# Performance work log

Hardware: AMD Instinct MI355X
Metric: run time of the kernel (lower is better)

The kernel has to match this reference:

```python
import jax, jax.numpy as jnp
import numpy as np

B, DIM, H, W = 8, 128, 128, 128
QK, MLP, HEADS, NT, GS = 128, 256, 4, 8, 128


def _ln(x, w, b):
    m = jnp.mean(x, -1, keepdims=True)
    v = jnp.mean((x - m) ** 2, -1, keepdims=True)
    return (x - m) * jax.lax.rsqrt(v + 1e-5) * w + b


def _norml2(x):
    n = jnp.sqrt(jnp.sum(x * x, -1, keepdims=True))
    return x / jnp.maximum(n, 1e-12)


def setup_inputs() -> dict:
    key = jax.random.key(0)
    ks = jax.random.split(key, 12)
    s = 0.02
    f32 = jnp.float32
    return {
        'x': jax.random.normal(ks[0], (B, DIM, H, W), f32),
        'means': jax.random.normal(ks[1], (NT, DIM), f32),
        'ln1_w': jnp.ones((DIM,), f32), 'ln1_b': jnp.zeros((DIM,), f32),
        'wq': jax.random.normal(ks[2], (QK, DIM), f32) * s,
        'wk': jax.random.normal(ks[3], (QK, DIM), f32) * s,
        'wv': jax.random.normal(ks[4], (DIM, DIM), f32) * s,
        'wproj': jax.random.normal(ks[5], (DIM, DIM), f32) * s,
        'irca_wk': jax.random.normal(ks[6], (QK, DIM), f32) * s,
        'irca_wv': jax.random.normal(ks[7], (DIM, DIM), f32) * s,
        'conv1x1_w': jax.random.normal(ks[8], (DIM, DIM), f32) * s,
        'ln2_w': jnp.ones((DIM,), f32), 'ln2_b': jnp.zeros((DIM,), f32),
        'fc1_w': jax.random.normal(ks[9], (MLP, DIM), f32) * s,
        'fc1_b': jnp.zeros((MLP,), f32),
        'dw_w': jax.random.normal(ks[10], (MLP, 1, 5, 5), f32) * s,
        'dw_b': jnp.zeros((MLP,), f32),
        'fc2_w': jax.random.normal(ks[11], (DIM, MLP), f32) * s,
        'fc2_b': jnp.zeros((DIM,), f32),
    }


def reference(x, means, ln1_w, ln1_b, wq, wk, wv, wproj, irca_wk, irca_wv,
              conv1x1_w, ln2_w, ln2_b, fc1_w, fc1_b, dw_w, dw_b, fc2_w, fc2_b):
    Bx, C, Hh, Ww = x.shape
    N = Hh * Ww
    xt = x.reshape(Bx, C, N).transpose(0, 2, 1)          # b n c
    residual = xt
    xn = _ln(xt, ln1_w, ln1_b)
    m = jax.lax.stop_gradient(means)                      # eval: means buffer, detached
    # IRCA (eval path): global K/V from cluster means
    dq, dv = QK // HEADS, C // HEADS
    kg = (m @ irca_wk.T).reshape(NT, HEADS, dq).transpose(1, 0, 2)  # h nt dq
    vg = (m @ irca_wv.T).reshape(NT, HEADS, dv).transpose(1, 0, 2)  # h nt dv
    # cluster assignment -> token reordering (no grad)
    scores = jnp.einsum('bic,jc->bij', _norml2(xn), _norml2(m))
    buckets = jnp.argmax(scores, axis=-1)
    idx = jnp.argsort(buckets, axis=-1)                   # [B,N] permutation
    # IASA
    q = xn @ wq.T
    k = xn @ wk.T
    v = xn @ wv.T
    take = lambda t: jnp.take_along_axis(t, idx[:, :, None], axis=1)
    q, k, v = take(q), take(k), take(v)
    gs = min(N, GS)
    ng = (N + gs - 1) // gs
    pad_n = ng * gs - N
    qp = jnp.concatenate([q, jnp.flip(q[:, N - pad_n:N], axis=1)], axis=1)
    qp = qp.reshape(Bx, ng, gs, HEADS, dq).transpose(0, 1, 3, 2, 4)  # b g h gs dq

    def window(t, d):
        tp = jnp.concatenate([t, jnp.flip(t[:, N - pad_n - gs:N], axis=1)], axis=1)
        blk = tp.reshape(Bx, ng + 1, gs, HEADS, d)
        win = jnp.concatenate([blk[:, :-1], blk[:, 1:]], axis=2)     # b g 2gs h d
        return win.transpose(0, 1, 3, 2, 4)

    kp = window(k, dq)
    vp = window(v, dv)
    scale = 1.0 / np.sqrt(dq)
    a1 = jax.nn.softmax(jnp.einsum('bghqd,bghkd->bghqk', qp, kp) * scale, axis=-1)
    out1 = jnp.einsum('bghqk,bghkd->bghqd', a1, vp)
    a2 = jax.nn.softmax(jnp.einsum('bghqd,hkd->bghqk', qp, kg) * scale, axis=-1)
    out2 = jnp.einsum('bghqk,hkd->bghqd', a2, vg)
    out = (out1 + out2).transpose(0, 1, 3, 2, 4).reshape(Bx, ng * gs, C)[:, :N]
    inv = jnp.argsort(idx, axis=-1)                       # scatter-back = inverse perm
    out = jnp.take_along_axis(out, inv[:, :, None], axis=1)
    out = out @ wproj.T
    yimg = out.transpose(0, 2, 1).reshape(Bx, C, Hh, Ww)
    yimg = jnp.einsum('oc,bchw->bohw', conv1x1_w, yimg)
    x2 = residual + yimg.reshape(Bx, C, N).transpose(0, 2, 1)
    # ConvFFN with PreNorm
    xm = _ln(x2, ln2_w, ln2_b)
    h1 = jax.nn.gelu(xm @ fc1_w.T + fc1_b, approximate=False)
    himg = h1.transpose(0, 2, 1).reshape(Bx, MLP, Hh, Ww)
    dwc = jax.lax.conv_general_dilated(himg, dw_w, (1, 1), 'SAME',
                                       feature_group_count=MLP,
                                       dimension_numbers=('NCHW', 'OIHW', 'NCHW'))
    dwc = jax.nn.gelu(dwc + dw_b.reshape(1, MLP, 1, 1), approximate=False)
    h1 = h1 + dwc.reshape(Bx, MLP, N).transpose(0, 2, 1)
    x3 = x2 + (h1 @ fc2_w.T + fc2_b)
    return x3.transpose(0, 2, 1).reshape(Bx, C, Hh, Ww)
```

## Files before the change

kernel.cpp:

```cpp
#include <hip/hip_runtime.h>
#include <math.h>

typedef unsigned short u16;
typedef unsigned int u32;
typedef __attribute__((ext_vector_type(8))) short bf16x8;
typedef __attribute__((ext_vector_type(4))) float f32x4;

constexpr int BB   = 8;
constexpr int DIMC = 128;
constexpr int HH   = 128;
constexpr int WW   = 128;
constexpr int NTOK = HH * WW;
constexpr int QKD  = 128;
constexpr int MLPD = 256;
constexpr int NTm  = 8;
constexpr int GSZ  = 128;
constexpr int NGRP = NTOK / GSZ;
constexpr size_t BIG = 16777216;

__device__ __forceinline__ float exp2_raw(float x) {
    return __builtin_amdgcn_exp2f(x);
}
__device__ __forceinline__ float gelu_f(float v) {
    float u = v * (0.7978845608028654f + 0.035677408136300125f * v * v);
    float e = exp2_raw(u * 2.885390081777927f);
    float th = 1.0f - 2.0f * __builtin_amdgcn_rcpf(e + 1.0f);
    return 0.5f * v * (1.0f + th);
}
__device__ __forceinline__ float b2f(u16 u) {
    return __uint_as_float(((u32)u) << 16);
}
__device__ __forceinline__ u16 f2b(float f) {
    u32 x = __float_as_uint(f);
    return (u16)((x + 0x7fffu + ((x >> 16) & 1u)) >> 16);
}
__device__ __forceinline__ float ulo(u32 u) { return __uint_as_float(u << 16); }
__device__ __forceinline__ float uhi(u32 u) { return __uint_as_float(u & 0xffff0000u); }

__global__ __launch_bounds__(128) void k_prep(const float* __restrict__ means,
        const float* __restrict__ iwk, const float* __restrict__ iwv,
        float* __restrict__ mhat, u16* __restrict__ kgbb, u16* __restrict__ vgtb) {
    __shared__ float sm[DIMC];
    __shared__ float inv_s;
    int tt = blockIdx.x;
    int t = threadIdx.x;
    sm[t] = means[tt * DIMC + t];
    __syncthreads();
    if (t == 0) {
        float s = 0.f;
        for (int c = 0; c < DIMC; c++) s += sm[c] * sm[c];
        inv_s = 1.f / fmaxf(sqrtf(s), 1e-12f);
    }
    __syncthreads();
    mhat[tt * DIMC + t] = sm[t] * inv_s;
    float sk = 0.f, sv = 0.f;
    #pragma unroll 8
    for (int c = 0; c < DIMC; c++) {
        sk = fmaf(sm[c], iwk[t * DIMC + c], sk);
        sv = fmaf(sm[c], iwv[t * DIMC + c], sv);
    }
    kgbb[tt * DIMC + t] = f2b(sk);
    vgtb[(t >> 5) * 256 + (t & 31) * 8 + tt] = f2b(sv);
}

__global__ __launch_bounds__(256) void k_cvtall(const float* __restrict__ wq,
        const float* __restrict__ wk, const float* __restrict__ wv,
        const float* __restrict__ fc1, const float* __restrict__ fc2,
        u16* __restrict__ wqkv, u16* __restrict__ fc1b, u16* __restrict__ fc2b) {
    int i = blockIdx.x * 256 + threadIdx.x;
    if (i < 49152) {
        const float* s = (i < 16384) ? wq : (i < 32768 ? wk : wv);
        wqkv[i] = f2b(s[i & 16383]);
    } else if (i < 81920) {
        fc1b[i - 49152] = f2b(fc1[i - 49152]);
    } else if (i < 114688) {
        fc2b[i - 81920] = f2b(fc2[i - 81920]);
    }
}

__global__ __launch_bounds__(256) void k_fuse(const float* __restrict__ c1,
        const float* __restrict__ wp, u16* __restrict__ wf) {
    __shared__ float wpS[DIMC * DIMC];
    int t = threadIdx.x;
    for (int i = t; i < DIMC * DIMC; i += 256) wpS[i] = wp[i];
    __syncthreads();
    int o = blockIdx.x * 2 + (t >> 7);
    int c = t & 127;
    float s = 0.f;
    #pragma unroll 8
    for (int m = 0; m < DIMC; m++) s = fmaf(c1[o * DIMC + m], wpS[m * DIMC + c], s);
    wf[o * DIMC + c] = f2b(s);
}

__global__ __launch_bounds__(256) void k_ln1(const float* __restrict__ x,
        const float* __restrict__ lw, const float* __restrict__ lb,
        const float* __restrict__ mhat, u16* __restrict__ xn, int* __restrict__ bucket) {
    __shared__ float smh[NTm * DIMC];
    __shared__ float lwb[DIMC], lbb[DIMC];
    __shared__ float red[4][64][3];
    __shared__ float scr[4][64][9];
    const int chunk = blockIdx.x;
    const int b = chunk >> 8;
    const int n0 = (chunk & 255) << 6;
    const int t = threadIdx.x;
    const int cg = t >> 6, tok = t & 63;
    const int n = n0 + tok;
    const int cbase = cg * 32;
    for (int i = t; i < NTm * DIMC; i += 256) smh[i] = mhat[i];
    if (t < DIMC) { lwb[t] = lw[t]; lbb[t] = lb[t]; }

    const float* xb = x + (size_t)b * DIMC * NTOK + (size_t)cbase * NTOK + n;
    float xv[32];
    float sum = 0.f, sq = 0.f;
    #pragma unroll
    for (int c = 0; c < 32; c++) {
        float v = xb[(size_t)c * NTOK];
        xv[c] = v;
        sum += v; sq += v * v;
    }
    red[cg][tok][0] = sum;
    red[cg][tok][1] = sq;
    __syncthreads();
    float s0 = red[0][tok][0] + red[1][tok][0] + red[2][tok][0] + red[3][tok][0];
    float q0 = red[0][tok][1] + red[1][tok][1] + red[2][tok][1] + red[3][tok][1];
    float mean = s0 * (1.0f / DIMC);
    float var = q0 * (1.0f / DIMC) - mean * mean;
    float rstd = rsqrtf(var + 1e-5f);

    float sc[NTm];
    #pragma unroll
    for (int j = 0; j < NTm; j++) sc[j] = 0.f;
    u32 opk[16];
    #pragma unroll
    for (int c = 0; c < 32; c += 2) {
        float v0 = (xv[c]     - mean) * rstd * lwb[cbase + c]     + lbb[cbase + c];
        float v1 = (xv[c + 1] - mean) * rstd * lwb[cbase + c + 1] + lbb[cbase + c + 1];
        #pragma unroll
        for (int j = 0; j < NTm; j++) {
            sc[j] = fmaf(v0, smh[j * DIMC + cbase + c], sc[j]);
            sc[j] = fmaf(v1, smh[j * DIMC + cbase + c + 1], sc[j]);
        }
        opk[c >> 1] = (u32)f2b(v0) | ((u32)f2b(v1) << 16);
    }
    u16* xnr = xn + ((size_t)b * NTOK + n) * DIMC + cbase;
    *(uint4*)(xnr + 0)  = make_uint4(opk[0],  opk[1],  opk[2],  opk[3]);
    *(uint4*)(xnr + 8)  = make_uint4(opk[4],  opk[5],  opk[6],  opk[7]);
    *(uint4*)(xnr + 16) = make_uint4(opk[8],  opk[9],  opk[10], opk[11]);
    *(uint4*)(xnr + 24) = make_uint4(opk[12], opk[13], opk[14], opk[15]);

    #pragma unroll
    for (int j = 0; j < NTm; j++) scr[cg][tok][j] = sc[j];
    __syncthreads();
    if (cg == 0) {
        float v0 = ((scr[0][tok][0] + scr[1][tok][0]) + (scr[2][tok][0] + scr[3][tok][0]));
        int best = 0; float bv = v0;
        #pragma unroll
        for (int j = 1; j < NTm; j++) {
            float v = ((scr[0][tok][j] + scr[1][tok][j]) + (scr[2][tok][j] + scr[3][tok][j]));
            if (v > bv) { bv = v; best = j; }
        }
        bucket[b * NTOK + n] = best;
    }
}

__global__ __launch_bounds__(64) void k_count(const int* __restrict__ bucket, int* __restrict__ cnt) {
    int chunk = blockIdx.x;
    int bk = bucket[(chunk << 6) + threadIdx.x];
    #pragma unroll
    for (int j = 0; j < NTm; j++) {
        unsigned long long m = __ballot(bk == j);
        if (threadIdx.x == 0) cnt[chunk * NTm + j] = (int)__popcll(m);
    }
}

__global__ __launch_bounds__(64) void k_scan(const int* __restrict__ cnt, int* __restrict__ base) {
    __shared__ int sc[256 * NTm];
    __shared__ int bb[NTm], tot[NTm];
    int b = blockIdx.x, t = threadIdx.x;
    for (int i = t; i < 256 * NTm; i += 64) sc[i] = cnt[b * 256 * NTm + i];
    __syncthreads();
    if (t < NTm) {
        int run = 0;
        for (int c = 0; c < 256; c++) {
            int v = sc[c * NTm + t];
            sc[c * NTm + t] = run;
            run += v;
        }
        tot[t] = run;
    }
    __syncthreads();
    if (t == 0) {
        int a = 0;
        for (int j = 0; j < NTm; j++) { bb[j] = a; a += tot[j]; }
    }
    __syncthreads();
    for (int i = t; i < 256 * NTm; i += 64) base[b * 256 * NTm + i] = sc[i] + bb[i & 7];
}

__global__ __launch_bounds__(64) void k_place(const int* __restrict__ bucket,
        const int* __restrict__ base, int* __restrict__ gidx) {
    int chunk = blockIdx.x;
    int lane = threadIdx.x;
    int nf = (chunk << 6) + lane;
    int bk = bucket[nf];
    unsigned long long lower = (1ull << lane) - 1ull;
    int rank = 0;
    #pragma unroll
    for (int j = 0; j < NTm; j++) {
        unsigned long long m = __ballot(bk == j);
        if (bk == j) rank = (int)__popcll(m & lower);
    }
    int b = nf >> 14;
    int pos = base[chunk * NTm + bk] + rank;
    gidx[b * NTOK + pos] = nf & (NTOK - 1);
}

__global__ __launch_bounds__(256) void k_inv(const int* __restrict__ gidx, u16* __restrict__ iinv) {
    int i = blockIdx.x * 256 + threadIdx.x;
    int b = i >> 14;
    iinv[((size_t)b << 14) + gidx[i]] = (u16)(i & (NTOK - 1));
}

template<int KDIM, int NOUT, int GATHER, int AIMG, int BIASF, int GELUF, int RES, int STIMG, int CBF, int LN2F>
__global__ __launch_bounds__(256) void g_mfma(const u16* __restrict__ A, const u16* __restrict__ W,
        const float* __restrict__ bias, const void* __restrict__ resid,
        const int* __restrict__ gidx, void* __restrict__ Cout, float ascale,
        const float* __restrict__ lnw, const float* __restrict__ lnb, void* __restrict__ Cout2) {
    __shared__ u16 As[128 * 40];
    __shared__ u16 Ws[128 * 40];
    const int b = blockIdx.z;
    const int m0 = blockIdx.x * 128;
    const int n0 = blockIdx.y * 128;
    const int t = threadIdx.x;
    const int lane = t & 63;
    const int wave = t >> 6;
    const int wm = (wave & 1) * 64;
    const int wn = (wave >> 1) * 64;
    const int srow = t >> 2;
    const int sko = (t & 3) * 8;
    const u16* pA0 = nullptr; const u16* pA1 = nullptr;
    if (!AIMG) {
        int ra0 = m0 + srow, ra1 = m0 + 64 + srow;
        if (GATHER == 1) {
            ra0 = gidx[b * NTOK + ra0];
            ra1 = gidx[b * NTOK + ra1];
        } else if (GATHER == 2) {
            const u16* gi = (const u16*)gidx;
            ra0 = gi[b * NTOK + ra0];
            ra1 = gi[b * NTOK + ra1];
        }
        pA0 = A + ((size_t)b * NTOK + ra0) * KDIM + sko;
        pA1 = A + ((size_t)b * NTOK + ra1) * KDIM + sko;
    }
    const u16* pW0 = W + (size_t)(n0 + srow) * KDIM + sko;
    const u16* pW1 = W + (size_t)(n0 + 64 + srow) * KDIM + sko;

    f32x4 acc[4][4];
    #pragma unroll
    for (int i = 0; i < 4; i++)
        #pragma unroll
        for (int j = 0; j < 4; j++) acc[i][j] = (f32x4){0.f, 0.f, 0.f, 0.f};

    uint4 a0c, a1c, w0c, w1c;
    u16 ec[16];
    if (!AIMG) {
        a0c = *(const uint4*)(pA0);
        a1c = *(const uint4*)(pA1);
    } else {
        const int kk2 = t & 31;
        const int tg = t >> 5;
        const u16* src = A + ((size_t)b * KDIM + kk2) * NTOK + m0 + tg * 16;
        *(uint4*)&ec[0] = *(const uint4*)src;
        *(uint4*)&ec[8] = *(const uint4*)(src + 8);
    }
    w0c = *(const uint4*)(pW0);
    w1c = *(const uint4*)(pW1);

    #pragma unroll
    for (int k0 = 0; k0 < KDIM; k0 += 32) {
        __syncthreads();
        if (!AIMG) {
            *(uint4*)&As[srow * 40 + sko] = a0c;
            *(uint4*)&As[(64 + srow) * 40 + sko] = a1c;
        } else {
            const int kk2 = t & 31;
            const int tg = t >> 5;
            #pragma unroll
            for (int j = 0; j < 16; j++) As[(tg * 16 + j) * 40 + kk2] = ec[j];
        }
        *(uint4*)&Ws[srow * 40 + sko] = w0c;
        *(uint4*)&Ws[(64 + srow) * 40 + sko] = w1c;
        __syncthreads();
        if (k0 + 32 < KDIM) {
            if (!AIMG) {
                a0c = *(const uint4*)(pA0 + k0 + 32);
                a1c = *(const uint4*)(pA1 + k0 + 32);
            } else {
                const int kk2 = t & 31;
                const int tg = t >> 5;
                const u16* src = A + ((size_t)b * KDIM + k0 + 32 + kk2) * NTOK + m0 + tg * 16;
                *(uint4*)&ec[0] = *(const uint4*)src;
                *(uint4*)&ec[8] = *(const uint4*)(src + 8);
            }
            w0c = *(const uint4*)(pW0 + k0 + 32);
            w1c = *(const uint4*)(pW1 + k0 + 32);
        }
        bf16x8 af[4], bfv[4];
        #pragma unroll
        for (int i = 0; i < 4; i++)
            af[i] = *(bf16x8*)&As[(wm + i * 16 + (lane & 15)) * 40 + (lane >> 4) * 8];
        #pragma unroll
        for (int j = 0; j < 4; j++)
            bfv[j] = *(bf16x8*)&Ws[(wn + j * 16 + (lane & 15)) * 40 + (lane >> 4) * 8];
        #pragma unroll
        for (int i = 0; i < 4; i++)
            #pragma unroll
            for (int j = 0; j < 4; j++)
                acc[i][j] = __builtin_amdgcn_mfma_f32_16x16x32_bf16(af[i], bfv[j], acc[i][j], 0, 0, 0);
    }

    const int c2 = lane & 15, gq2 = lane >> 4;
    int colj[4];
    #pragma unroll
    for (int j = 0; j < 4; j++) colj[j] = n0 + wn + j * 16 + c2;

    if (LN2F) {
        #pragma unroll
        for (int i = 0; i < 4; i++) {
            int rbase = m0 + wm + i * 16 + gq2 * 4;
            #pragma unroll
            for (int j = 0; j < 4; j++) {
                const float* rf = (const float*)resid;
                float4 rr = *(const float4*)&rf[((size_t)b * NOUT + colj[j]) * NTOK + rbase];
                acc[i][j][0] += rr.x; acc[i][j][1] += rr.y;
                acc[i][j][2] += rr.z; acc[i][j][3] += rr.w;
            }
        }
        __syncthreads();
        float* ps = (float*)&As[0];
        const int h = wn >> 6;
        float mean_[4][4], rstd_[4][4];
        #pragma unroll
        for (int i = 0; i < 4; i++)
            #pragma unroll
            for (int r = 0; r < 4; r++) {
                float s = 0.f, q = 0.f;
                #pragma unroll
                for (int j = 0; j < 4; j++) { float tv = acc[i][j][r]; s += tv; q += tv * tv; }
                s += __shfl_xor(s, 1, 64); q += __shfl_xor(q, 1, 64);
                s += __shfl_xor(s, 2, 64); q += __shfl_xor(q, 2, 64);
                s += __shfl_xor(s, 4, 64); q += __shfl_xor(q, 4, 64);
                s += __shfl_xor(s, 8, 64); q += __shfl_xor(q, 8, 64);
                if (c2 == 0) {
                    int rl = wm + i * 16 + gq2 * 4 + r;
                    ps[(h * 128 + rl) * 2 + 0] = s;
                    ps[(h * 128 + rl) * 2 + 1] = q;
                }
            }
        __syncthreads();
        #pragma unroll
        for (int i = 0; i < 4; i++)
            #pragma unroll
            for (int r = 0; r < 4; r++) {
                int rl = wm + i * 16 + gq2 * 4 + r;
                float s = ps[rl * 2 + 0] + ps[(128 + rl) * 2 + 0];
                float q = ps[rl * 2 + 1] + ps[(128 + rl) * 2 + 1];
                float mn = s * (1.0f / 128.0f);
                float vr = q * (1.0f / 128.0f) - mn * mn;
                mean_[i][r] = mn;
                rstd_[i][r] = rsqrtf(vr + 1e-5f);
            }
        float lwj[4], lbj[4];
        #pragma unroll
        for (int j = 0; j < 4; j++) { lwj[j] = lnw[colj[j]]; lbj[j] = lnb[colj[j]]; }
        u16* xo = (u16*)Cout;
        u16* mo = (u16*)Cout2;
        #pragma unroll
        for (int i = 0; i < 4; i++) {
            int rbase = m0 + wm + i * 16 + gq2 * 4;
            #pragma unroll
            for (int j = 0; j < 4; j++)
                #pragma unroll
                for (int r = 0; r < 4; r++) {
                    float tv = acc[i][j][r];
                    size_t off = ((size_t)b * NTOK + rbase + r) * NOUT + colj[j];
                    xo[off] = f2b(tv);
                    mo[off] = f2b((tv - mean_[i][r]) * rstd_[i][r] * lwj[j] + lbj[j]);
                }
        }
        return;
    }

    const float smul = (blockIdx.y == 0) ? ascale : 1.0f;
    float bj[4];
    #pragma unroll
    for (int j = 0; j < 4; j++) bj[j] = BIASF ? bias[colj[j]] : 0.f;
    #pragma unroll
    for (int i = 0; i < 4; i++) {
        int rbase = m0 + wm + i * 16 + gq2 * 4;
        #pragma unroll
        for (int j = 0; j < 4; j++) {
            f32x4 v = acc[i][j];
            v[0] *= smul; v[1] *= smul; v[2] *= smul; v[3] *= smul;
            if (BIASF) { v[0] += bj[j]; v[1] += bj[j]; v[2] += bj[j]; v[3] += bj[j]; }
            if (GELUF) { v[0] = gelu_f(v[0]); v[1] = gelu_f(v[1]); v[2] = gelu_f(v[2]); v[3] = gelu_f(v[3]); }
            if (RES == 1) {
                const float* rf = (const float*)resid;
                float4 rr = *(const float4*)&rf[((size_t)b * NOUT + colj[j]) * NTOK + rbase];
                v[0] += rr.x; v[1] += rr.y; v[2] += rr.z; v[3] += rr.w;
            } else if (RES == 3) {
                const u16* rb = (const u16*)resid;
                #pragma unroll
                for (int r = 0; r < 4; r++)
                    v[r] += b2f(rb[((size_t)b * NTOK + rbase + r) * NOUT + colj[j]]);
            }
            if (STIMG) {
                size_t off = ((size_t)b * NOUT + colj[j]) * NTOK + rbase;
                if (CBF) {
                    ushort4 o;
                    o.x = f2b(v[0]); o.y = f2b(v[1]); o.z = f2b(v[2]); o.w = f2b(v[3]);
                    *(ushort4*)((u16*)Cout + off) = o;
                } else {
                    *(float4*)((float*)Cout + off) = make_float4(v[0], v[1], v[2], v[3]);
                }
            } else {
                if (CBF) {
                    #pragma unroll
                    for (int r = 0; r < 4; r++)
                        ((u16*)Cout)[((size_t)b * NTOK + rbase + r) * NOUT + colj[j]] = f2b(v[r]);
                } else {
                    #pragma unroll
                    for (int r = 0; r < 4; r++)
                        ((float*)Cout)[((size_t)b * NTOK + rbase + r) * NOUT + colj[j]] = v[r];
                }
            }
        }
    }
}

__global__ __launch_bounds__(256, 3) void k_attn(const u16* __restrict__ qkv,
        const u16* __restrict__ kgbb, const u16* __restrict__ vgtb,
        u16* __restrict__ outp) {
    __shared__ u16 VT[2][32][264];
    __shared__ u16 Pb[4][64][32];
    const int g = blockIdx.x, hp = blockIdx.y, b = blockIdx.z;
    const int t = threadIdx.x;
    const int wave = t >> 6, lane = t & 63;
    const int c = lane & 15, gq = lane >> 4;
    const int lh = wave & 1, head = hp * 2 + lh, qh = wave >> 1;
    const size_t brow = (size_t)b * NTOK;
    const bool lastg = (g == NGRP - 1);
    const int csw = (c & 3) << 3;

    {
        int key = t;
        int pos = (!lastg || key < GSZ) ? g * GSZ + key : NTOK - 1 - (key - GSZ);
        const u16* vp = qkv + (brow + pos) * 384 + 256 + hp * 64;
        #pragma unroll
        for (int i = 0; i < 8; i++) {
            uint4 v = *(const uint4*)(vp + i * 8);
            u16 e[8];
            *(uint4*)e = v;
            #pragma unroll
            for (int j = 0; j < 8; j++) {
                int d = i * 8 + j;
                VT[d >> 5][d & 31][key] = e[j];
            }
        }
        if (t < 64) {
            int l2 = t >> 5, dv = t & 31;
            uint4 v = *(const uint4*)(vgtb + ((size_t)(hp * 2 + l2) * 32 + dv) * 8);
            *(uint4*)&VT[l2][dv][256] = v;
        }
    }

    const int q0 = g * GSZ + qh * 64;
    bf16x8 qf[4];
    #pragma unroll
    for (int nq = 0; nq < 4; nq++)
        qf[nq] = *(const bf16x8*)(qkv + (brow + q0 + nq * 16 + c) * 384 + head * 32 + gq * 8);

    const u16* kbp = qkv + brow * 384 + 128 + head * 32 + gq * 8;
    bf16x8 kfa[8][2];
    #pragma unroll
    for (int s = 0; s < 8; s++)
        #pragma unroll
        for (int mk = 0; mk < 2; mk++) {
            int kl = s * 32 + mk * 16 + c;
            int pos = (!lastg || kl < GSZ) ? g * GSZ + kl : NTOK - 1 - (kl - GSZ);
            kfa[s][mk] = *(const bf16x8*)(kbp + (size_t)pos * 384);
        }
    bf16x8 kgf = *(const bf16x8*)(kgbb + (c & 7) * 128 + head * 32 + gq * 8);

    __syncthreads();

    f32x4 acc[4][2];
    #pragma unroll
    for (int i = 0; i < 4; i++)
        #pragma unroll
        for (int j = 0; j < 2; j++) acc[i][j] = (f32x4){0.f, 0.f, 0.f, 0.f};
    float lsum[4] = {0.f, 0.f, 0.f, 0.f};

    for (int s = 0; s < 8; s++) {
        #pragma unroll
        for (int mk = 0; mk < 2; mk++) {
            #pragma unroll
            for (int nq = 0; nq < 4; nq++) {
                f32x4 st = __builtin_amdgcn_mfma_f32_16x16x32_bf16(kfa[s][mk], qf[nq],
                        (f32x4){0.f, 0.f, 0.f, 0.f}, 0, 0, 0);
                float p0 = exp2_raw(st[0]), p1 = exp2_raw(st[1]);
                float p2 = exp2_raw(st[2]), p3 = exp2_raw(st[3]);
                lsum[nq] += (p0 + p1) + (p2 + p3);
                u32 r0, r1;
                asm("v_cvt_pk_bf16_f32 %0, %1, %2" : "=v"(r0) : "v"(p0), "v"(p1));
                asm("v_cvt_pk_bf16_f32 %0, %1, %2" : "=v"(r1) : "v"(p2), "v"(p3));
                *(uint2*)&Pb[wave][nq * 16 + c][(mk * 16 + gq * 4) ^ csw] = make_uint2(r0, r1);
            }
        }
        __builtin_amdgcn_sched_barrier(0);
        bf16x8 pf[4], vf[2];
        #pragma unroll
        for (int mt = 0; mt < 4; mt++)
            pf[mt] = *(const bf16x8*)&Pb[wave][mt * 16 + c][(gq * 8) ^ csw];
        #pragma unroll
        for (int nv = 0; nv < 2; nv++)
            vf[nv] = *(const bf16x8*)&VT[lh][nv * 16 + c][s * 32 + gq * 8];
        #pragma unroll
        for (int mt = 0; mt < 4; mt++)
            #pragma unroll
            for (int nv = 0; nv < 2; nv++)
                acc[mt][nv] = __builtin_amdgcn_mfma_f32_16x16x32_bf16(pf[mt], vf[nv], acc[mt][nv], 0, 0, 0);
    }

    #pragma unroll
    for (int nq = 0; nq < 4; nq++) {
        lsum[nq] += __shfl_xor(lsum[nq], 16, 64);
        lsum[nq] += __shfl_xor(lsum[nq], 32, 64);
    }

    {
        #pragma unroll
        for (int nq = 0; nq < 4; nq++) {
            f32x4 sg = __builtin_amdgcn_mfma_f32_16x16x32_bf16(kgf, qf[nq],
                    (f32x4){0.f, 0.f, 0.f, 0.f}, 0, 0, 0);
            float p0, p1, p2, p3;
            if (gq < 2) {
                p0 = exp2_raw(sg[0]); p1 = exp2_raw(sg[1]);
                p2 = exp2_raw(sg[2]); p3 = exp2_raw(sg[3]);
            } else { p0 = p1 = p2 = p3 = 0.f; }
            float lg = (p0 + p1) + (p2 + p3);
            lg += __shfl_xor(lg, 16, 64);
            lg += __shfl_xor(lg, 32, 64);
            float w = lsum[nq] / lg;
            p0 *= w; p1 *= w; p2 *= w; p3 *= w;
            u32 r0, r1;
            asm("v_cvt_pk_bf16_f32 %0, %1, %2" : "=v"(r0) : "v"(p0), "v"(p1));
            asm("v_cvt_pk_bf16_f32 %0, %1, %2" : "=v"(r1) : "v"(p2), "v"(p3));
            *(uint2*)&Pb[wave][nq * 16 + c][(gq * 4) ^ csw] = make_uint2(r0, r1);
        }
        __builtin_amdgcn_sched_barrier(0);
        bf16x8 zf;
        #pragma unroll
        for (int z8 = 0; z8 < 8; z8++) zf[z8] = 0;
        bf16x8 pf[4], vf[2];
        #pragma unroll
        for (int mt = 0; mt < 4; mt++)
            pf[mt] = *(const bf16x8*)&Pb[wave][mt * 16 + c][(gq * 8) ^ csw];
        #pragma unroll
        for (int nv = 0; nv < 2; nv++)
            vf[nv] = (gq == 0) ? *(const bf16x8*)&VT[lh][nv * 16 + c][256] : zf;
        #pragma unroll
        for (int mt = 0; mt < 4; mt++)
            #pragma unroll
            for (int nv = 0; nv < 2; nv++)
                acc[mt][nv] = __builtin_amdgcn_mfma_f32_16x16x32_bf16(pf[mt], vf[nv], acc[mt][nv], 0, 0, 0);
    }

    float* lf = (float*)&Pb[wave][0][0];
    if (gq == 0) {
        #pragma unroll
        for (int nq = 0; nq < 4; nq++) lf[nq * 16 + c] = lsum[nq];
    }
    __builtin_amdgcn_sched_barrier(0);
    u16 ov[4][2][4];
    #pragma unroll
    for (int mt = 0; mt < 4; mt++) {
        float il[4];
        #pragma unroll
        for (int r = 0; r < 4; r++)
            il[r] = 1.f / lf[mt * 16 + gq * 4 + r];
        #pragma unroll
        for (int nv = 0; nv < 2; nv++)
            #pragma unroll
            for (int r = 0; r < 4; r++)
                ov[mt][nv][r] = f2b(acc[mt][nv][r] * il[r]);
    }

    __syncthreads();
    u16* st = (u16*)&VT[0][0][0];
    #pragma unroll
    for (int mt = 0; mt < 4; mt++)
        #pragma unroll
        for (int nv = 0; nv < 2; nv++)
            #pragma unroll
            for (int r = 0; r < 4; r++)
                st[(qh * 64 + mt * 16 + gq * 4 + r) * 68 + lh * 32 + nv * 16 + c] = ov[mt][nv][r];
    __syncthreads();
    {
        const int rl0 = t >> 3;
        const int seg = t & 7;
        #pragma unroll
        for (int p = 0; p < 4; p++) {
            int rl = rl0 + p * 32;
            uint4 v4 = *(const uint4*)&st[rl * 68 + seg * 8];
            *(uint4*)&outp[(brow + g * GSZ + rl) * 128 + hp * 64 + seg * 8] = v4;
        }
    }
}

__global__ __launch_bounds__(256) void k_dw(const u16* __restrict__ himg,
        const float* __restrict__ dww, const float* __restrict__ dwb, u16* __restrict__ dsum) {
    const int mc = blockIdx.y, b = blockIdx.z;
    const int t = threadIdx.x;
    const int y = blockIdx.x * 32 + (t >> 4) * 2;
    const int xb = (t & 15) * 8;
    float wgt[25];
    #pragma unroll
    for (int i = 0; i < 25; i++) wgt[i] = dww[mc * 25 + i];
    const float bsv = dwb[mc];
    const u16* src = himg + ((size_t)b * MLPD + mc) * NTOK;
    u16* dst = dsum + ((size_t)b * MLPD + mc) * NTOK;

    float w[6][12];
    #pragma unroll
    for (int r = 0; r < 6; r++) {
        int ysrc = y - 2 + r;
        bool vy = (ysrc >= 0 && ysrc < HH);
        const u16* rp = src + ysrc * WW + xb;
        uint4 aq = vy ? *(const uint4*)(rp - 8) : make_uint4(0u, 0u, 0u, 0u);
        uint4 bq = vy ? *(const uint4*)(rp)     : make_uint4(0u, 0u, 0u, 0u);
        uint4 cq = vy ? *(const uint4*)(rp + 8) : make_uint4(0u, 0u, 0u, 0u);
        w[r][0]  = ulo(aq.w); w[r][1]  = uhi(aq.w);
        w[r][2]  = ulo(bq.x); w[r][3]  = uhi(bq.x);
        w[r][4]  = ulo(bq.y); w[r][5]  = uhi(bq.y);
        w[r][6]  = ulo(bq.z); w[r][7]  = uhi(bq.z);
        w[r][8]  = ulo(bq.w); w[r][9]  = uhi(bq.w);
        w[r][10] = ulo(cq.x); w[r][11] = uhi(cq.x);
        if (xb == 0)   { w[r][0]  = 0.f; w[r][1]  = 0.f; }
        if (xb == 120) { w[r][10] = 0.f; w[r][11] = 0.f; }
    }

    float acc0[8], acc1[8];
    #pragma unroll
    for (int px = 0; px < 8; px++) { acc0[px] = 0.f; acc1[px] = 0.f; }
    #pragma unroll
    for (int dy = 0; dy < 5; dy++)
        #pragma unroll
        for (int dx = 0; dx < 5; dx++) {
            float wv = wgt[dy * 5 + dx];
            #pragma unroll
            for (int px = 0; px < 8; px++) {
                acc0[px] = fmaf(wv, w[dy][px + dx], acc0[px]);
                acc1[px] = fmaf(wv, w[dy + 1][px + dx], acc1[px]);
            }
        }

    u32 o0[4], o1[4];
    #pragma unroll
    for (int px = 0; px < 8; px += 2) {
        u16 a0 = f2b(w[2][px + 2] + gelu_f(acc0[px] + bsv));
        u16 a1 = f2b(w[2][px + 3] + gelu_f(acc0[px + 1] + bsv));
        o0[px >> 1] = (u32)a0 | ((u32)a1 << 16);
        u16 b0 = f2b(w[3][px + 2] + gelu_f(acc1[px] + bsv));
        u16 b1 = f2b(w[3][px + 3] + gelu_f(acc1[px + 1] + bsv));
        o1[px >> 1] = (u32)b0 | ((u32)b1 << 16);
    }
    *(uint4*)(dst + y * WW + xb) = *(uint4*)o0;
    *(uint4*)(dst + (y + 1) * WW + xb) = *(uint4*)o1;
}

extern "C" void kernel_launch(void* const* d_in, const int* in_sizes, int n_in,
                              void* d_out, int out_size, void* d_ws, size_t ws_size,
                              hipStream_t stream) {
    const float* x       = (const float*)d_in[0];
    const float* means   = (const float*)d_in[1];
    const float* ln1_w   = (const float*)d_in[2];
    const float* ln1_b   = (const float*)d_in[3];
    const float* wq      = (const float*)d_in[4];
    const float* wk      = (const float*)d_in[5];
    const float* wv      = (const float*)d_in[6];
    const float* wproj   = (const float*)d_in[7];
    const float* irca_wk = (const float*)d_in[8];
    const float* irca_wv = (const float*)d_in[9];
    const float* conv1w  = (const float*)d_in[10];
    const float* ln2_w   = (const float*)d_in[11];
    const float* ln2_b   = (const float*)d_in[12];
    const float* fc1_w   = (const float*)d_in[13];
    const float* fc1_b   = (const float*)d_in[14];
    const float* dw_w    = (const float*)d_in[15];
    const float* dw_b    = (const float*)d_in[16];
    const float* fc2_w   = (const float*)d_in[17];
    const float* fc2_b   = (const float*)d_in[18];
    float* out = (float*)d_out;

    const size_t need = 202514432;
    if (ws_size < need) return;

    char* base = (char*)d_ws;
    float* mhat  = (float*)(base);
    u16*   kgbb  = (u16*)(base + 4096);
    u16*   vgtb  = (u16*)(base + 6144);
    int*   bucket = (int*)(base + 8192);
    u16*   wqkv  = (u16*)(base + 8192);
    u16*   wfub  = wqkv + 3 * 16384;
    u16*   fc1b  = wfub + 16384;
    u16*   fc2b  = fc1b + 32768;
    u16*   iinv  = (u16*)(base + 270336);
    int*   cnt   = (int*)(base + 532480);
    int*   cbase = (int*)(base + 598016);
    int*   gidx  = (int*)(base + 663552);
    u16*   Abase = (u16*)(base + 1187840);
    u16*   x2b   = (u16*)(base + 101851136);
    u16*   dsum  = (u16*)(base + 135405568);

    u16* qkv  = Abase;
    u16* himg = Abase;
    u16* xmb  = Abase + 2 * BIG;
    u16* xnb   = (u16*)d_out;
    u16* attnb = (u16*)d_out;

    k_prep<<<NTm, 128, 0, stream>>>(means, irca_wk, irca_wv, mhat, kgbb, vgtb);
    k_ln1<<<BB * NTOK / 64, 256, 0, stream>>>(x, ln1_w, ln1_b, mhat, xnb, bucket);
    k_count<<<BB * NTOK / 64, 64, 0, stream>>>(bucket, cnt);
    k_scan<<<BB, 64, 0, stream>>>(cnt, cbase);
    k_place<<<BB * NTOK / 64, 64, 0, stream>>>(bucket, cbase, gidx);
    k_inv<<<BB * NTOK / 256, 256, 0, stream>>>(gidx, iinv);

    k_cvtall<<<448, 256, 0, stream>>>(wq, wk, wv, fc1_w, fc2_w, wqkv, fc1b, fc2b);
    k_fuse<<<64, 256, 0, stream>>>(conv1w, wproj, wfub);

    const float qsc2 = 0.25503489924160945f;
    g_mfma<128, 384, 1, 0, 0, 0, 0, 0, 1, 0><<<dim3(128, 3, BB), 256, 0, stream>>>(
        xnb, wqkv, nullptr, nullptr, gidx, qkv, qsc2, nullptr, nullptr, nullptr);

    k_attn<<<dim3(NGRP, 2, BB), 256, 0, stream>>>(qkv, kgbb, vgtb, attnb);

    g_mfma<128, 128, 2, 0, 0, 0, 1, 0, 1, 1><<<dim3(128, 1, BB), 256, 0, stream>>>(
        attnb, wfub, nullptr, x, (const int*)iinv, x2b, 1.0f, ln2_w, ln2_b, xmb);

    g_mfma<128, 256, 0, 0, 1, 1, 0, 1, 1, 0><<<dim3(128, 2, BB), 256, 0, stream>>>(
        xmb, fc1b, fc1_b, nullptr, nullptr, himg, 1.0f, nullptr, nullptr, nullptr);
    k_dw<<<dim3(4, MLPD, BB), 256, 0, stream>>>(himg, dw_w, dw_b, dsum);
    g_mfma<256, 128, 0, 1, 1, 0, 3, 1, 0, 0><<<dim3(128, 1, BB), 256, 0, stream>>>(
        dsum, fc2b, fc2_b, x2b, nullptr, out, 1.0f, nullptr, nullptr, nullptr);

    (void)in_sizes; (void)n_in; (void)out_size;
}
```

Baseline: 294.8 us.

## Load GEMM operand fragments directly from global memory, bypassing LDS staging

For row-major A inputs (not the image-layout path), the GEMM kernel now has each lane load its MFMA fragments straight from global memory into registers, with a one-step register prefetch, and no longer stages tiles through shared memory with barriers. Shared memory arrays are sized per template so non-image variants allocate little LDS, which may raise occupancy. In exchange, A and W rows are read redundantly by different waves (each wave reads its 64x128 slice), relying on cache instead of LDS reuse, and the global loads are less coalesced.

```diff
diff --git a/kernel.cpp b/kernel.cpp
--- a/kernel.cpp
+++ b/kernel.cpp
@@ -226,8 +226,8 @@
         const float* __restrict__ bias, const void* __restrict__ resid,
         const int* __restrict__ gidx, void* __restrict__ Cout, float ascale,
         const float* __restrict__ lnw, const float* __restrict__ lnb, void* __restrict__ Cout2) {
-    __shared__ u16 As[128 * 40];
-    __shared__ u16 Ws[128 * 40];
+    __shared__ u16 As[AIMG ? 128 * 40 : (LN2F ? 1024 : 4)];
+    __shared__ u16 Ws[AIMG ? 128 * 40 : 4];
     const int b = blockIdx.z;
     const int m0 = blockIdx.x * 128;
     const int n0 = blockIdx.y * 128;
@@ -236,24 +236,7 @@
     const int wave = t >> 6;
     const int wm = (wave & 1) * 64;
     const int wn = (wave >> 1) * 64;
-    const int srow = t >> 2;
-    const int sko = (t & 3) * 8;
-    const u16* pA0 = nullptr; const u16* pA1 = nullptr;
-    if (!AIMG) {
-        int ra0 = m0 + srow, ra1 = m0 + 64 + srow;
-        if (GATHER == 1) {
-            ra0 = gidx[b * NTOK + ra0];
-            ra1 = gidx[b * NTOK + ra1];
-        } else if (GATHER == 2) {
-            const u16* gi = (const u16*)gidx;
-            ra0 = gi[b * NTOK + ra0];
-            ra1 = gi[b * NTOK + ra1];
-        }
-        pA0 = A + ((size_t)b * NTOK + ra0) * KDIM + sko;
-        pA1 = A + ((size_t)b * NTOK + ra1) * KDIM + sko;
-    }
-    const u16* pW0 = W + (size_t)(n0 + srow) * KDIM + sko;
-    const u16* pW1 = W + (size_t)(n0 + 64 + srow) * KDIM + sko;
+    const int c2 = lane & 15, gq2 = lane >> 4;
 
     f32x4 acc[4][4];
     #pragma unroll
@@ -261,65 +244,90 @@
         #pragma unroll
         for (int j = 0; j < 4; j++) acc[i][j] = (f32x4){0.f, 0.f, 0.f, 0.f};
 
-    uint4 a0c, a1c, w0c, w1c;
-    u16 ec[16];
-    if (!AIMG) {
-        a0c = *(const uint4*)(pA0);
-        a1c = *(const uint4*)(pA1);
-    } else {
+    if (AIMG) {
+        const int srow = t >> 2;
+        const int sko = (t & 3) * 8;
         const int kk2 = t & 31;
         const int tg = t >> 5;
-        const u16* src = A + ((size_t)b * KDIM + kk2) * NTOK + m0 + tg * 16;
-        *(uint4*)&ec[0] = *(const uint4*)src;
-        *(uint4*)&ec[8] = *(const uint4*)(src + 8);
-    }
-    w0c = *(const uint4*)(pW0);
-    w1c = *(const uint4*)(pW1);
-
-    #pragma unroll
-    for (int k0 = 0; k0 < KDIM; k0 += 32) {
-        __syncthreads();
-        if (!AIMG) {
-            *(uint4*)&As[srow * 40 + sko] = a0c;
-            *(uint4*)&As[(64 + srow) * 40 + sko] = a1c;
-        } else {
-            const int kk2 = t & 31;
-            const int tg = t >> 5;
+        const u16* pW0 = W + (size_t)(n0 + srow) * KDIM + sko;
+        const u16* pW1 = W + (size_t)(n0 + 64 + srow) * KDIM + sko;
+        uint4 w0c, w1c;
+        u16 ec[16];
+        {
+            const u16* src = A + ((size_t)b * KDIM + kk2) * NTOK + m0 + tg * 16;
+            *(uint4*)&ec[0] = *(const uint4*)src;
+            *(uint4*)&ec[8] = *(const uint4*)(src + 8);
+            w0c = *(const uint4*)(pW0);
+            w1c = *(const uint4*)(pW1);
+        }
+        #pragma unroll
+        for (int k0 = 0; k0 < KDIM; k0 += 32) {
+            __syncthreads();
             #pragma unroll
             for (int j = 0; j < 16; j++) As[(tg * 16 + j) * 40 + kk2] = ec[j];
-        }
-        *(uint4*)&Ws[srow * 40 + sko] = w0c;
-        *(uint4*)&Ws[(64 + srow) * 40 + sko] = w1c;
-        __syncthreads();
-        if (k0 + 32 < KDIM) {
-            if (!AIMG) {
-                a0c = *(const uint4*)(pA0 + k0 + 32);
-                a1c = *(const uint4*)(pA1 + k0 + 32);
-            } else {
-                const int kk2 = t & 31;
-                const int tg = t >> 5;
+            *(uint4*)&Ws[srow * 40 + sko] = w0c;
+            *(uint4*)&Ws[(64 + srow) * 40 + sko] = w1c;
+            __syncthreads();
+            if (k0 + 32 < KDIM) {
                 const u16* src = A + ((size_t)b * KDIM + k0 + 32 + kk2) * NTOK + m0 + tg * 16;
                 *(uint4*)&ec[0] = *(const uint4*)src;
                 *(uint4*)&ec[8] = *(const uint4*)(src + 8);
-            }
-            w0c = *(const uint4*)(pW0 + k0 + 32);
-            w1c = *(const uint4*)(pW1 + k0 + 32);
-        }
-        bf16x8 af[4], bfv[4];
-        #pragma unroll
-        for (int i = 0; i < 4; i++)
-            af[i] = *(bf16x8*)&As[(wm + i * 16 + (lane & 15)) * 40 + (lane >> 4) * 8];
+                w0c = *(const uint4*)(pW0 + k0 + 32);
+                w1c = *(const uint4*)(pW1 + k0 + 32);
+            }
+            bf16x8 af[4], bfv[4];
+            #pragma unroll
+            for (int i = 0; i < 4; i++)
+                af[i] = *(bf16x8*)&As[(wm + i * 16 + c2) * 40 + gq2 * 8];
+            #pragma unroll
+            for (int j = 0; j < 4; j++)
+                bfv[j] = *(bf16x8*)&Ws[(wn + j * 16 + c2) * 40 + gq2 * 8];
+            #pragma unroll
+            for (int i = 0; i < 4; i++)
+                #pragma unroll
+                for (int j = 0; j < 4; j++)
+                    acc[i][j] = __builtin_amdgcn_mfma_f32_16x16x32_bf16(af[i], bfv[j], acc[i][j], 0, 0, 0);
+        }
+    } else {
+        const u16* aP[4];
+        const u16* wP[4];
+        #pragma unroll
+        for (int i = 0; i < 4; i++) {
+            int r = m0 + wm + i * 16 + c2;
+            if (GATHER == 1) r = gidx[b * NTOK + r];
+            else if (GATHER == 2) r = ((const u16*)gidx)[b * NTOK + r];
+            aP[i] = A + ((size_t)b * NTOK + r) * KDIM + gq2 * 8;
+        }
         #pragma unroll
         for (int j = 0; j < 4; j++)
-            bfv[j] = *(bf16x8*)&Ws[(wn + j * 16 + (lane & 15)) * 40 + (lane >> 4) * 8];
-        #pragma unroll
-        for (int i = 0; i < 4; i++)
-            #pragma unroll
-            for (int j = 0; j < 4; j++)
-                acc[i][j] = __builtin_amdgcn_mfma_f32_16x16x32_bf16(af[i], bfv[j], acc[i][j], 0, 0, 0);
-    }
-
-    const int c2 = lane & 15, gq2 = lane >> 4;
+            wP[j] = W + (size_t)(n0 + wn + j * 16 + c2) * KDIM + gq2 * 8;
+
+        bf16x8 afc[4], bfc[4];
+        #pragma unroll
+        for (int i = 0; i < 4; i++) afc[i] = *(const bf16x8*)(aP[i]);
+        #pragma unroll
+        for (int j = 0; j < 4; j++) bfc[j] = *(const bf16x8*)(wP[j]);
+        #pragma unroll
+        for (int ks = 0; ks < KDIM / 32; ks++) {
+            bf16x8 af[4], bfv[4];
+            #pragma unroll
+            for (int i = 0; i < 4; i++) af[i] = afc[i];
+            #pragma unroll
+            for (int j = 0; j < 4; j++) bfv[j] = bfc[j];
+            if (ks + 1 < KDIM / 32) {
+                #pragma unroll
+                for (int i = 0; i < 4; i++) afc[i] = *(const bf16x8*)(aP[i] + (ks + 1) * 32);
+                #pragma unroll
+                for (int j = 0; j < 4; j++) bfc[j] = *(const bf16x8*)(wP[j] + (ks + 1) * 32);
+            }
+            #pragma unroll
+            for (int i = 0; i < 4; i++)
+                #pragma unroll
+                for (int j = 0; j < 4; j++)
+                    acc[i][j] = __builtin_amdgcn_mfma_f32_16x16x32_bf16(af[i], bfv[j], acc[i][j], 0, 0, 0);
+        }
+    }
+
     int colj[4];
     #pragma unroll
     for (int j = 0; j < 4; j++) colj[j] = n0 + wn + j * 16 + c2;
```

New measurement: 337.8 us. 1.15x slower.
